# Kernel tuning notes

Hardware: AMD Instinct MI355X
Metric: run time of the kernel (lower is better)

The kernel has to match this reference:

```python
import jax, jax.numpy as jnp
import numpy as np

N = 50000    # num_nodes
E = 800000   # num_edges
IN = 256     # input_dim
H = 256      # hidden_dim
EPS = 1e-5   # BatchNorm eps


def setup_inputs() -> dict:
    key = jax.random.key(0)
    ks = jax.random.split(key, 12)
    def nrm(k, shp, s=0.05):
        return jax.random.normal(k, shp, dtype=jnp.float32) * s
    return {
        "x": jax.random.normal(ks[0], (N, IN), dtype=jnp.float32),
        "edge_index": jax.random.randint(ks[1], (2, E), 0, N, dtype=jnp.int32),
        "edge_weight": jax.random.uniform(ks[2], (E,), dtype=jnp.float32),
        # GCNConv 1 / 2 (PyG stores weight as [in, out]; bias [out])
        "W1": nrm(ks[3], (IN, H)), "b1": jnp.zeros((H,), jnp.float32),
        "W2": nrm(ks[4], (H, H)), "b2": jnp.zeros((H,), jnp.float32),
        # BatchNorm1d 1 / 2
        "gamma1": jnp.ones((H,), jnp.float32), "beta1": jnp.zeros((H,), jnp.float32),
        "gamma2": jnp.ones((H,), jnp.float32), "beta2": jnp.zeros((H,), jnp.float32),
        # LSTM 1 (input 2H) and LSTM 2 (input H), PyTorch gate order i,f,g,o
        "Wih1": nrm(ks[5], (4 * H, 2 * H)), "Whh1": nrm(ks[6], (4 * H, H)),
        "bih1": jnp.zeros((4 * H,), jnp.float32), "bhh1": jnp.zeros((4 * H,), jnp.float32),
        "Wih2": nrm(ks[7], (4 * H, H)), "Whh2": nrm(ks[8], (4 * H, H)),
        "bih2": jnp.zeros((4 * H,), jnp.float32), "bhh2": jnp.zeros((4 * H,), jnp.float32),
    }


def reference(x, edge_index, edge_weight, W1, b1, W2, b2, gamma1, beta1,
              gamma2, beta2, Wih1, Whh1, bih1, bhh1, Wih2, Whh2, bih2, bhh2):
    src, dst = edge_index[0], edge_index[1]
    # GCN symmetric normalization with added self-loops (fill value 1.0)
    loops = jnp.arange(N, dtype=src.dtype)
    src_a = jnp.concatenate([src, loops])
    dst_a = jnp.concatenate([dst, loops])
    ew_a = jnp.concatenate([edge_weight, jnp.ones((N,), edge_weight.dtype)])
    deg = jax.ops.segment_sum(ew_a, dst_a, num_segments=N)
    deg_safe = jnp.where(deg > 0, deg, 1.0)
    dinv = jnp.where(deg > 0, jax.lax.rsqrt(deg_safe), 0.0)
    norm = dinv[src_a] * ew_a * dinv[dst_a]  # [E+N]

    def gcn(h, W, b):
        m = (h @ W)[src_a] * norm[:, None]               # gather + scale messages
        return jax.ops.segment_sum(m, dst_a, num_segments=N) + b

    def bn(h, g, bta):  # training-mode BatchNorm1d (batch stats, biased var)
        mu = jnp.mean(h, axis=0)
        var = jnp.mean((h - mu) ** 2, axis=0)
        return (h - mu) * jax.lax.rsqrt(var + EPS) * g + bta

    def lstm_step0(inp, Wih, bih, bhh):  # single step from h0=c0=0 (window=1)
        gates = inp @ Wih.T + bih + bhh  # Whh term vanishes since h0=0
        i, f, g, o = jnp.split(gates, 4, axis=-1)
        c = jax.nn.sigmoid(i) * jnp.tanh(g)  # f*c0 = 0
        return jax.nn.sigmoid(o) * jnp.tanh(c)

    h1 = bn(jax.nn.relu(gcn(x, W1, b1)), gamma1, beta1)   # [N, H]
    h2 = bn(jax.nn.relu(gcn(h1, W2, b2)), gamma2, beta2)  # [N, H]
    Xc = jnp.concatenate([h1, h2], axis=1)                # [N, 2H]
    hL1 = lstm_step0(Xc, Wih1, bih1, bhh1)                # LSTM1 final hidden
    hL2 = lstm_step0(hL1, Wih2, bih2, bhh2)               # LSTM2 final hidden
    # S with window=1 reduces to x itself
    return jnp.concatenate([hL1, hL2, x], axis=1)         # [N, 2H + IN]
```

## Files before the change

### kernel.cpp

```cpp
#include <hip/hip_runtime.h>
#include <math.h>

#define NN 50000
#define NE 800000

typedef __attribute__((ext_vector_type(8))) short bf8;
typedef __attribute__((ext_vector_type(4))) float f32x4;
typedef unsigned int u32;
typedef unsigned long long u64;

__device__ __forceinline__ unsigned short f2b(float f){
  union{float f;unsigned u;} v; v.f=f;
  unsigned r=v.u+0x7fff+((v.u>>16)&1u);
  return (unsigned short)(r>>16);
}
__device__ __forceinline__ float b2f(unsigned short h){
  union{unsigned u;float f;} v; v.u=((unsigned)h)<<16; return v.f;
}
__device__ __forceinline__ float lo_bf(u32 t){ union{u32 u;float f;} v; v.u=t<<16; return v.f; }
__device__ __forceinline__ float hi_bf(u32 t){ union{u32 u;float f;} v; v.u=t&0xffff0000u; return v.f; }
__device__ __forceinline__ float fsigm(float x){ return __builtin_amdgcn_rcpf(1.f+__expf(-x)); }
__device__ __forceinline__ float ftanh(float x){ return 1.f-2.f*__builtin_amdgcn_rcpf(__expf(2.f*x)+1.f); }

__device__ __forceinline__ void gload16(const unsigned short* g, unsigned short* l){
  __builtin_amdgcn_global_load_lds((const __attribute__((address_space(1))) u32*)g,
                                   (__attribute__((address_space(3))) u32*)l,
                                   16,0,0);
}

__device__ __forceinline__ int wscan_incl(int v,int lane){
  #pragma unroll
  for(int d=1;d<64;d<<=1){ int t=__shfl_up(v,d,64); if(lane>=d)v+=t; }
  return v;
}

__global__ __launch_bounds__(256) void k_init(float* deg,int* cnt,float* colsum,float* colsq){
  int i=blockIdx.x*256+threadIdx.x;
  if(i<NN){deg[i]=1.0f;cnt[i]=0;}
  if(i<256){colsum[i]=0.f;colsq[i]=0.f;}
}

__global__ __launch_bounds__(256) void k_deg(const int* __restrict__ ei,const float* __restrict__ ew,
                                             float* deg,int* cnt){
  int e=blockIdx.x*256+threadIdx.x;
  if(e<NE){int d=ei[NE+e];atomicAdd(&deg[d],ew[e]);atomicAdd(&cnt[d],1);}
}

__global__ __launch_bounds__(256) void k_dinv(const float* __restrict__ deg,float* dinv){
  int i=blockIdx.x*256+threadIdx.x;
  if(i<NN){float d=deg[i];dinv[i]=d>0.f?rsqrtf(d):0.f;}
}

__global__ __launch_bounds__(1024) void k_scan1(const int* __restrict__ cnt,int* row_ptr,int* bsum){
  __shared__ int wsum[16];
  __shared__ int woff[17];
  int tid=threadIdx.x,lane=tid&63,w=tid>>6;
  int i=blockIdx.x*1024+tid;
  int v=(i<NN)?cnt[i]:0;
  int incl=wscan_incl(v,lane);
  if(lane==63)wsum[w]=incl;
  __syncthreads();
  if(w==0){
    int t=(lane<16)?wsum[lane]:0;
    int s=wscan_incl(t,lane);
    if(lane<16)woff[lane+1]=s;
    if(lane==0)woff[0]=0;
  }
  __syncthreads();
  int excl=incl-v+woff[w];
  if(i<NN)row_ptr[i]=excl;
  if(tid==0)bsum[blockIdx.x]=woff[16];
}
__global__ __launch_bounds__(64) void k_scan2(int* bsum,int* bbase,int* row_ptr,int nblk){
  int tid=threadIdx.x;
  int v=(tid<nblk)?bsum[tid]:0;
  int incl=wscan_incl(v,tid);
  bbase[tid]=incl-v;
  if(tid==63)row_ptr[NN]=incl;
}
__global__ __launch_bounds__(256) void k_scan3(int* row_ptr,int* cursor,const int* __restrict__ bbase){
  int i=blockIdx.x*256+threadIdx.x;
  if(i<NN){
    int r=row_ptr[i]+bbase[i>>10];
    row_ptr[i]=r;cursor[i]=r;
  }
}

__global__ __launch_bounds__(256) void k_scatter(const int* __restrict__ ei,const float* __restrict__ ew,
    const float* __restrict__ dinv,int* cursor,int2* csr_sw){
  int e=blockIdx.x*256+threadIdx.x;
  if(e<NE){
    int s=ei[e],d=ei[NE+e];
    float wv=dinv[s]*ew[e]*dinv[d];
    int p=atomicAdd(&cursor[d],1);
    int2 o;o.x=s;o.y=__float_as_int(wv);
    csr_sw[p]=o;
  }
}

__global__ __launch_bounds__(256) void k_wt(const float* __restrict__ W,unsigned short* __restrict__ Wt){
  int j=blockIdx.x,k=threadIdx.x;
  Wt[j*256+k]=f2b(W[k*256+j]);
}
__global__ __launch_bounds__(256) void k_f2b(const float* __restrict__ s,unsigned short* __restrict__ d,int n){
  int i=blockIdx.x*256+threadIdx.x;
  if(i<n)d[i]=f2b(s[i]);
}
__global__ __launch_bounds__(256) void k_cast(const float* __restrict__ s,unsigned short* __restrict__ d){
  long i=(long)blockIdx.x*256+threadIdx.x;
  float4 v=*(const float4*)&s[i*4];
  ushort4 o;o.x=f2b(v.x);o.y=f2b(v.y);o.z=f2b(v.z);o.w=f2b(v.w);
  *(ushort4*)&d[i*4]=o;
}
__global__ __launch_bounds__(256) void k_bsum(const float* __restrict__ a,const float* __restrict__ b,
                                              float* __restrict__ s,int n){
  int i=blockIdx.x*256+threadIdx.x;
  if(i<n)s[i]=a[i]+b[i];
}

__global__ __launch_bounds__(256) void k_foldw(const float* __restrict__ W,
    const float* __restrict__ scale,const float* __restrict__ shift,
    unsigned short* __restrict__ Wt,float* __restrict__ tw){
  __shared__ float red[256];
  int j=blockIdx.x,k=threadIdx.x;
  float w=W[k*256+j];
  Wt[j*256+k]=f2b(w*scale[k]);
  red[k]=w*shift[k];
  __syncthreads();
  for(int off=128;off>0;off>>=1){ if(k<off)red[k]+=red[k+off]; __syncthreads(); }
  if(k==0)tw[j]=red[0];
}

__global__ __launch_bounds__(256) void k_foldlstm(const float* __restrict__ Wih,int K,
    const float* __restrict__ scale,const float* __restrict__ shift,
    const float* __restrict__ bih,const float* __restrict__ bhh,
    unsigned short* __restrict__ Wb,float* __restrict__ bs){
  __shared__ float red[256];
  int m=blockIdx.x,t=threadIdx.x;
  float part=0.f;
  for(int k=t;k<K;k+=256){
    float w=Wih[(long)m*K+k];
    Wb[(long)m*K+k]=f2b(w*scale[k]);
    part+=w*shift[k];
  }
  red[t]=part;
  __syncthreads();
  for(int off=128;off>0;off>>=1){ if(t<off)red[t]+=red[t+off]; __syncthreads(); }
  if(t==0)bs[m]=bih[m]+bhh[m]+red[0];
}

__global__ __launch_bounds__(256,2) void k_gemm_mfma(
    const unsigned short* __restrict__ A,int lda,const unsigned short* __restrict__ Bt,int K,
    unsigned short* __restrict__ Cb){
  __shared__ unsigned short As[2][4096];
  __shared__ unsigned short Bs[2][4096];
  int tid=threadIdx.x;
  int row0=blockIdx.x*128,col0=blockIdx.y*128;
  int lane=tid&63,l15=lane&15,quad=lane>>4;
  int wid=tid>>6,wm=wid>>1,wn=wid&1;
  int sr=tid>>2;
  int aoff=((tid&3)^((tid>>3)&3))*8;
  int xq=quad^((l15>>1)&3);
  long ar0=row0+sr;    if(ar0>=NN)ar0=NN-1;
  long ar1=row0+64+sr; if(ar1>=NN)ar1=NN-1;
  const unsigned short* a0p=A+ar0*lda+aoff;
  const unsigned short* a1p=A+ar1*lda+aoff;
  const unsigned short* b0p=Bt+(long)(col0+sr)*K+aoff;
  const unsigned short* b1p=Bt+(long)(col0+64+sr)*K+aoff;
  int lb=wid*512;
  f32x4 acc[4][4]={};
  int nt=K/32;
  gload16(a0p,&As[0][lb]); gload16(a1p,&As[0][2048+lb]);
  gload16(b0p,&Bs[0][lb]); gload16(b1p,&Bs[0][2048+lb]);
  __syncthreads();
  for(int t=0;t<nt;t++){
    int cur=t&1;
    if(t+1<nt){
      int k0=(t+1)*32;int nxt=cur^1;
      gload16(a0p+k0,&As[nxt][lb]); gload16(a1p+k0,&As[nxt][2048+lb]);
      gload16(b0p+k0,&Bs[nxt][lb]); gload16(b1p+k0,&Bs[nxt][2048+lb]);
    }
    bf8 af[4],bfg[4];
    #pragma unroll
    for(int i=0;i<4;i++){
      af[i] =*(const bf8*)&As[cur][(wm*64+i*16+l15)*32+xq*8];
      bfg[i]=*(const bf8*)&Bs[cur][(wn*64+i*16+l15)*32+xq*8];
    }
    #pragma unroll
    for(int mi=0;mi<4;mi++)
      #pragma unroll
      for(int ni=0;ni<4;ni++)
        acc[mi][ni]=__builtin_amdgcn_mfma_f32_16x16x32_bf16(af[mi],bfg[ni],acc[mi][ni],0,0,0);
    __syncthreads();
  }
  #pragma unroll
  for(int mi=0;mi<4;mi++){
    #pragma unroll
    for(int r=0;r<4;r++){
      int node=row0+wm*64+mi*16+quad*4+r;
      if(node>=NN)continue;
      #pragma unroll
      for(int ni=0;ni<4;ni++){
        int col=col0+wn*64+ni*16+l15;
        Cb[((size_t)(col>>5)*NN+node)*32+(col&31)]=f2b(acc[mi][ni][r]);
      }
    }
  }
}

__global__ __launch_bounds__(256,2) void k_lstm_mfma(
    const unsigned short* __restrict__ A,int lda,int K,
    const unsigned short* __restrict__ Wb,const float* __restrict__ bsum,
    float* __restrict__ Hout,int ldh,unsigned short* __restrict__ Hb){
  __shared__ unsigned short As[2][4096];
  __shared__ unsigned short Bs[2][6144];
  int tid=threadIdx.x;
  int row0=blockIdx.x*128,m0=blockIdx.y*64;
  int lane=tid&63,l15=lane&15,quad=lane>>4;
  int wid=tid>>6,wm=wid>>1,wn=wid&1;
  int sr=tid>>2;
  int aoff=((tid&3)^((tid>>3)&3))*8;
  int xq=quad^((l15>>1)&3);
  long ar0=row0+sr;    if(ar0>=NN)ar0=NN-1;
  long ar1=row0+64+sr; if(ar1>=NN)ar1=NN-1;
  const unsigned short* a0p=A+ar0*lda+aoff;
  const unsigned short* a1p=A+ar1*lda+aoff;
  const unsigned short* wip=Wb+(long)(    m0+sr)*K+aoff;
  const unsigned short* wgp=Wb+(long)(512+m0+sr)*K+aoff;
  const unsigned short* wop=Wb+(long)(768+m0+sr)*K+aoff;
  int lb=wid*512;
  f32x4 ai[4][2]={},ag[4][2]={},ao[4][2]={};
  int nt=K/32;
  gload16(a0p,&As[0][lb]); gload16(a1p,&As[0][2048+lb]);
  gload16(wip,&Bs[0][lb]); gload16(wgp,&Bs[0][2048+lb]); gload16(wop,&Bs[0][4096+lb]);
  __syncthreads();
  for(int t=0;t<nt;t++){
    int cur=t&1;
    if(t+1<nt){
      int k0=(t+1)*32;int nxt=cur^1;
      gload16(a0p+k0,&As[nxt][lb]); gload16(a1p+k0,&As[nxt][2048+lb]);
      gload16(wip+k0,&Bs[nxt][lb]); gload16(wgp+k0,&Bs[nxt][2048+lb]); gload16(wop+k0,&Bs[nxt][4096+lb]);
    }
    bf8 af[4],bi[2],bg[2],bo[2];
    #pragma unroll
    for(int i=0;i<4;i++)af[i]=*(const bf8*)&As[cur][(wm*64+i*16+l15)*32+xq*8];
    #pragma unroll
    for(int ni=0;ni<2;ni++){
      int rr=wn*32+ni*16+l15;
      bi[ni]=*(const bf8*)&Bs[cur][(    rr)*32+xq*8];
      bg[ni]=*(const bf8*)&Bs[cur][( 64+rr)*32+xq*8];
      bo[ni]=*(const bf8*)&Bs[cur][(128+rr)*32+xq*8];
    }
    #pragma unroll
    for(int mi=0;mi<4;mi++)
      #pragma unroll
      for(int ni=0;ni<2;ni++){
        ai[mi][ni]=__builtin_amdgcn_mfma_f32_16x16x32_bf16(af[mi],bi[ni],ai[mi][ni],0,0,0);
        ag[mi][ni]=__builtin_amdgcn_mfma_f32_16x16x32_bf16(af[mi],bg[ni],ag[mi][ni],0,0,0);
        ao[mi][ni]=__builtin_amdgcn_mfma_f32_16x16x32_bf16(af[mi],bo[ni],ao[mi][ni],0,0,0);
      }
    __syncthreads();
  }
  #pragma unroll
  for(int ni=0;ni<2;ni++){
    int m=m0+wn*32+ni*16+l15;
    float b_i=bsum[m],b_g=bsum[512+m],b_o=bsum[768+m];
    #pragma unroll
    for(int mi=0;mi<4;mi++){
      #pragma unroll
      for(int r=0;r<4;r++){
        int node=row0+wm*64+mi*16+quad*4+r;
        if(node>=NN)continue;
        float gi=ai[mi][ni][r]+b_i;
        float gg=ag[mi][ni][r]+b_g;
        float go=ao[mi][ni][r]+b_o;
        float c=fsigm(gi)*ftanh(gg);
        float h=fsigm(go)*ftanh(c);
        Hout[(long)node*ldh+m]=h;
        if(Hb)Hb[(long)node*256+m]=f2b(h);
      }
    }
  }
}

__global__ __launch_bounds__(256) void k_spmm8(const unsigned short* __restrict__ T8,
    const int* __restrict__ row_ptr,const int2* __restrict__ csr_sw,
    const float* __restrict__ dinv,const float* __restrict__ bias,const float* __restrict__ tw,
    unsigned short* __restrict__ Xb,float* colsum,float* colsq){
  __shared__ float4 s_red[4][16];
  int tid=threadIdx.x;
  int lane=tid&63,wv=tid>>6;
  int g=lane>>4,li=lane&15;
  int chunk=blockIdx.x&7;
  int rowblk=blockIdx.x>>3;
  int r=rowblk*16+wv*4+g;
  int li2=li*2;
  int c0=chunk*32+li2;
  const unsigned short* Tc=T8+(size_t)chunk*NN*32;
  int p0=row_ptr[r],p1=row_ptr[r+1];
  int len=p1-p0;
  float di=dinv[r],ws=di*di;
  float rs=ws;
  u32 ts=*(const u32*)&Tc[(size_t)r*32+li2];
  float acc0=ws*lo_bf(ts),acc1=ws*hi_bf(ts);
  int Lm=len;
  Lm=max(Lm,__shfl_xor(Lm,16,64));
  Lm=max(Lm,__shfl_xor(Lm,32,64));
  for(int j=0;j<Lm;j+=4){
    #pragma unroll
    for(int u=0;u<4;u++){
      int jj=j+u;
      bool act=jj<len;
      int idx=p0+(act?jj:0);
      idx=min(idx,NE-1);
      u64 ev=__builtin_nontemporal_load((const u64*)&csr_sw[idx]);
      int s=(int)(u32)ev;
      float wgt=act?__int_as_float((int)(ev>>32)):0.f;
      s=min(max(s,0),NN-1);
      u32 t=*(const u32*)&Tc[(size_t)s*32+li2];
      acc0+=wgt*lo_bf(t);
      acc1+=wgt*hi_bf(t);
      rs+=wgt;
    }
  }
  float tw0=0.f,tw1=0.f;
  if(tw){ float2 tc=*(const float2*)&tw[c0]; tw0=tc.x; tw1=tc.y; }
  float2 bc=*(const float2*)&bias[c0];
  float a0=fmaxf(acc0+rs*tw0+bc.x,0.f);
  float a1=fmaxf(acc1+rs*tw1+bc.y,0.f);
  u32 o=(u32)f2b(a0)|((u32)f2b(a1)<<16);
  __builtin_nontemporal_store(o,(u32*)&Xb[(size_t)r*512+c0]);
  float s0=a0,s1=a1,q0=a0*a0,q1=a1*a1;
  #pragma unroll
  for(int m=16;m<=32;m<<=1){
    s0+=__shfl_xor(s0,m,64); s1+=__shfl_xor(s1,m,64);
    q0+=__shfl_xor(q0,m,64); q1+=__shfl_xor(q1,m,64);
  }
  if(lane<16)s_red[wv][lane]=make_float4(s0,s1,q0,q1);
  __syncthreads();
  if(tid<16){
    float4 a=s_red[0][tid],b=s_red[1][tid],c=s_red[2][tid],d=s_red[3][tid];
    float f0=a.x+b.x+c.x+d.x;
    float f1=a.y+b.y+c.y+d.y;
    float f2=a.z+b.z+c.z+d.z;
    float f3=a.w+b.w+c.w+d.w;
    int cc=chunk*32+tid*2;
    atomicAdd(&colsum[cc],f0);atomicAdd(&colsum[cc+1],f1);
    atomicAdd(&colsq[cc],f2);atomicAdd(&colsq[cc+1],f3);
  }
}

__global__ __launch_bounds__(256) void k_bnfin(const float* __restrict__ gamma,const float* __restrict__ beta,
    float* colsum,float* colsq,float* scale,float* shift){
  int c=threadIdx.x;
  float mu=colsum[c]/(float)NN;
  float var=colsq[c]/(float)NN-mu*mu;
  float r=rsqrtf(var+1e-5f);
  float sc=r*gamma[c];
  scale[c]=sc;
  shift[c]=beta[c]-mu*sc;
  colsum[c]=0.f;colsq[c]=0.f;
}

__global__ __launch_bounds__(256) void k_copy_out(const float* __restrict__ src,
    float* __restrict__ out,int colofs){
  long idx=(long)blockIdx.x*256+threadIdx.x;
  long r=idx>>6;int cc=(int)(idx&63)*4;
  if(r<NN)*(float4*)&out[r*768+colofs+cc]=*(const float4*)&src[r*256+cc];
}

extern "C" void kernel_launch(void* const* d_in,const int* in_sizes,int n_in,
                              void* d_out,int out_size,void* d_ws,size_t ws_size,
                              hipStream_t stream){
  const float* x   =(const float*)d_in[0];
  const int*   ei  =(const int*)  d_in[1];
  const float* ew  =(const float*)d_in[2];
  const float* W1  =(const float*)d_in[3];
  const float* b1  =(const float*)d_in[4];
  const float* W2  =(const float*)d_in[5];
  const float* b2  =(const float*)d_in[6];
  const float* g1  =(const float*)d_in[7];
  const float* be1 =(const float*)d_in[8];
  const float* g2  =(const float*)d_in[9];
  const float* be2 =(const float*)d_in[10];
  const float* Wih1=(const float*)d_in[11];
  const float* bih1=(const float*)d_in[13];
  const float* bhh1=(const float*)d_in[14];
  const float* Wih2=(const float*)d_in[15];
  const float* bih2=(const float*)d_in[17];
  const float* bhh2=(const float*)d_in[18];
  float* out=(float*)d_out;

  char* w=(char*)d_ws;
  auto alloc=[&](size_t bytes)->char*{char* p=w;w+=(bytes+255)&~(size_t)255;return p;};
  float* deg    =(float*)alloc((size_t)NN*4);
  float* dinv   =(float*)alloc((size_t)NN*4);
  int*   cnt    =(int*)  alloc((size_t)NN*4);
  int*   row_ptr=(int*)  alloc((size_t)(NN+1)*4);
  int*   cursor =(int*)  alloc((size_t)NN*4);
  int2*  csr_sw =(int2*) alloc((size_t)NE*8);
  int*   bsum_s =(int*)  alloc(64*4);
  int*   bbase  =(int*)  alloc(64*4);
  float* colsum =(float*)alloc(256*4);
  float* colsq  =(float*)alloc(256*4);
  float* scale  =(float*)alloc(512*4);
  float* shift  =(float*)alloc(512*4);
  float* tw     =(float*)alloc(256*4);
  unsigned short* Xcb =(unsigned short*)alloc((size_t)NN*512*2);
  unsigned short* TbH =(unsigned short*)alloc((size_t)NN*256*2);
  unsigned short* xb  =(unsigned short*)alloc((size_t)NN*256*2);
  unsigned short* Wt1 =(unsigned short*)alloc(256*256*2);
  unsigned short* Wt2 =(unsigned short*)alloc(256*256*2);
  unsigned short* Wb1 =(unsigned short*)alloc((size_t)1024*512*2);
  unsigned short* Wb2 =(unsigned short*)alloc((size_t)1024*256*2);
  float* bs1 =(float*)alloc(1024*4);
  float* bs2 =(float*)alloc(1024*4);

  int nb=(NN+255)/256;
  int nsc=(NN+1023)/1024;
  k_init<<<nb,256,0,stream>>>(deg,cnt,colsum,colsq);
  k_deg<<<(NE+255)/256,256,0,stream>>>(ei,ew,deg,cnt);
  k_dinv<<<nb,256,0,stream>>>(deg,dinv);
  k_scan1<<<nsc,1024,0,stream>>>(cnt,row_ptr,bsum_s);
  k_scan2<<<1,64,0,stream>>>(bsum_s,bbase,row_ptr,nsc);
  k_scan3<<<nb,256,0,stream>>>(row_ptr,cursor,bbase);
  k_scatter<<<(NE+255)/256,256,0,stream>>>(ei,ew,dinv,cursor,csr_sw);

  k_wt<<<256,256,0,stream>>>(W1,Wt1);
  k_cast<<<12500,256,0,stream>>>(x,xb);
  k_f2b<<<(1024*256+255)/256,256,0,stream>>>(Wih2,Wb2,1024*256);
  k_bsum<<<4,256,0,stream>>>(bih2,bhh2,bs2,1024);

  int ngx=(NN+127)/128;
  dim3 gd(ngx,2);
  dim3 gl(ngx,4);
  int nspmm=8*(NN/16);

  k_gemm_mfma<<<gd,256,0,stream>>>(xb,256,Wt1,256,TbH);
  k_spmm8<<<nspmm,256,0,stream>>>(TbH,row_ptr,csr_sw,dinv,b1,nullptr,Xcb+0,colsum,colsq);
  k_bnfin<<<1,256,0,stream>>>(g1,be1,colsum,colsq,scale,shift);
  k_foldw<<<256,256,0,stream>>>(W2,scale,shift,Wt2,tw);
  k_gemm_mfma<<<gd,256,0,stream>>>(Xcb,512,Wt2,256,TbH);
  k_spmm8<<<nspmm,256,0,stream>>>(TbH,row_ptr,csr_sw,dinv,b2,tw,Xcb+256,colsum,colsq);
  k_bnfin<<<1,256,0,stream>>>(g2,be2,colsum,colsq,scale+256,shift+256);
  k_foldlstm<<<1024,256,0,stream>>>(Wih1,512,scale,shift,bih1,bhh1,Wb1,bs1);
  k_lstm_mfma<<<gl,256,0,stream>>>(Xcb,512,512,Wb1,bs1,out+0,768,TbH);
  k_lstm_mfma<<<gl,256,0,stream>>>(TbH,256,256,Wb2,bs2,out+256,768,nullptr);
  k_copy_out<<<12500,256,0,stream>>>(x,out,512);
}
```

Baseline: 884.7 us.

## Widen SpMM gather to 16-byte loads with four lanes per row

```diff
diff --git a/kernel.cpp b/kernel.cpp
--- a/kernel.cpp
+++ b/kernel.cpp
@@ -17,8 +17,6 @@
 __device__ __forceinline__ float b2f(unsigned short h){
   union{unsigned u;float f;} v; v.u=((unsigned)h)<<16; return v.f;
 }
-__device__ __forceinline__ float lo_bf(u32 t){ union{u32 u;float f;} v; v.u=t<<16; return v.f; }
-__device__ __forceinline__ float hi_bf(u32 t){ union{u32 u;float f;} v; v.u=t&0xffff0000u; return v.f; }
 __device__ __forceinline__ float fsigm(float x){ return __builtin_amdgcn_rcpf(1.f+__expf(-x)); }
 __device__ __forceinline__ float ftanh(float x){ return 1.f-2.f*__builtin_amdgcn_rcpf(__expf(2.f*x)+1.f); }
 
@@ -287,66 +285,88 @@
     const int* __restrict__ row_ptr,const int2* __restrict__ csr_sw,
     const float* __restrict__ dinv,const float* __restrict__ bias,const float* __restrict__ tw,
     unsigned short* __restrict__ Xb,float* colsum,float* colsq){
-  __shared__ float4 s_red[4][16];
+  __shared__ float s_sum[4][32];
+  __shared__ float s_sq[4][32];
   int tid=threadIdx.x;
   int lane=tid&63,wv=tid>>6;
-  int g=lane>>4,li=lane&15;
+  int g=lane>>2,li=lane&3;
   int chunk=blockIdx.x&7;
   int rowblk=blockIdx.x>>3;
-  int r=rowblk*16+wv*4+g;
-  int li2=li*2;
-  int c0=chunk*32+li2;
+  int r=rowblk*64+wv*16+g;
+  bool valid=r<NN;
+  int rc=valid?r:0;
+  int co=li*8;
+  int c0=chunk*32+co;
   const unsigned short* Tc=T8+(size_t)chunk*NN*32;
-  int p0=row_ptr[r],p1=row_ptr[r+1];
-  int len=p1-p0;
-  float di=dinv[r],ws=di*di;
+  int p0=row_ptr[rc],p1=row_ptr[rc+1];
+  int len=valid?(p1-p0):0;
+  float di=dinv[rc],ws=di*di;
   float rs=ws;
-  u32 ts=*(const u32*)&Tc[(size_t)r*32+li2];
-  float acc0=ws*lo_bf(ts),acc1=ws*hi_bf(ts);
-  int Lm=len;
-  Lm=max(Lm,__shfl_xor(Lm,16,64));
-  Lm=max(Lm,__shfl_xor(Lm,32,64));
-  for(int j=0;j<Lm;j+=4){
-    #pragma unroll
-    for(int u=0;u<4;u++){
-      int jj=j+u;
-      bool act=jj<len;
-      int idx=p0+(act?jj:0);
-      idx=min(idx,NE-1);
-      u64 ev=__builtin_nontemporal_load((const u64*)&csr_sw[idx]);
-      int s=(int)(u32)ev;
-      float wgt=act?__int_as_float((int)(ev>>32)):0.f;
-      s=min(max(s,0),NN-1);
-      u32 t=*(const u32*)&Tc[(size_t)s*32+li2];
-      acc0+=wgt*lo_bf(t);
-      acc1+=wgt*hi_bf(t);
-      rs+=wgt;
-    }
-  }
-  float tw0=0.f,tw1=0.f;
-  if(tw){ float2 tc=*(const float2*)&tw[c0]; tw0=tc.x; tw1=tc.y; }
-  float2 bc=*(const float2*)&bias[c0];
-  float a0=fmaxf(acc0+rs*tw0+bc.x,0.f);
-  float a1=fmaxf(acc1+rs*tw1+bc.y,0.f);
-  u32 o=(u32)f2b(a0)|((u32)f2b(a1)<<16);
-  __builtin_nontemporal_store(o,(u32*)&Xb[(size_t)r*512+c0]);
-  float s0=a0,s1=a1,q0=a0*a0,q1=a1*a1;
+  float acc[8];
+  { bf8 t=*(const bf8*)&Tc[(u32)rc*32+co];
+    #pragma unroll
+    for(int e=0;e<8;e++)acc[e]=ws*b2f((unsigned short)t[e]);
+  }
+  int j=0;
+  for(;j+2<=len;j+=2){
+    u64 ev0=__builtin_nontemporal_load((const u64*)&csr_sw[p0+j]);
+    u64 ev1=__builtin_nontemporal_load((const u64*)&csr_sw[p0+j+1]);
+    int s0=(int)(u32)ev0; float w0=__int_as_float((int)(ev0>>32));
+    int s1=(int)(u32)ev1; float w1=__int_as_float((int)(ev1>>32));
+    s0=min(max(s0,0),NN-1); s1=min(max(s1,0),NN-1);
+    bf8 t0=*(const bf8*)&Tc[(u32)s0*32+co];
+    bf8 t1=*(const bf8*)&Tc[(u32)s1*32+co];
+    #pragma unroll
+    for(int e=0;e<8;e++)acc[e]+=w0*b2f((unsigned short)t0[e]);
+    #pragma unroll
+    for(int e=0;e<8;e++)acc[e]+=w1*b2f((unsigned short)t1[e]);
+    rs+=w0+w1;
+  }
+  if(j<len){
+    u64 ev=__builtin_nontemporal_load((const u64*)&csr_sw[p0+j]);
+    int s=(int)(u32)ev; float wg=__int_as_float((int)(ev>>32));
+    s=min(max(s,0),NN-1);
+    bf8 t=*(const bf8*)&Tc[(u32)s*32+co];
+    #pragma unroll
+    for(int e=0;e<8;e++)acc[e]+=wg*b2f((unsigned short)t[e]);
+    rs+=wg;
+  }
+  float4 bA=*(const float4*)&bias[c0],bB=*(const float4*)&bias[c0+4];
+  float4 tA=make_float4(0.f,0.f,0.f,0.f),tB=tA;
+  if(tw){ tA=*(const float4*)&tw[c0]; tB=*(const float4*)&tw[c0+4]; }
+  float o[8];
+  o[0]=fmaxf(acc[0]+rs*tA.x+bA.x,0.f);
+  o[1]=fmaxf(acc[1]+rs*tA.y+bA.y,0.f);
+  o[2]=fmaxf(acc[2]+rs*tA.z+bA.z,0.f);
+  o[3]=fmaxf(acc[3]+rs*tA.w+bA.w,0.f);
+  o[4]=fmaxf(acc[4]+rs*tB.x+bB.x,0.f);
+  o[5]=fmaxf(acc[5]+rs*tB.y+bB.y,0.f);
+  o[6]=fmaxf(acc[6]+rs*tB.z+bB.z,0.f);
+  o[7]=fmaxf(acc[7]+rs*tB.w+bB.w,0.f);
+  if(valid){
+    bf8 ov;
+    #pragma unroll
+    for(int e=0;e<8;e++)ov[e]=(short)f2b(o[e]);
+    __builtin_nontemporal_store(ov,(bf8*)&Xb[(size_t)r*512+c0]);
+  }
+  float sv[8],qv[8];
   #pragma unroll
-  for(int m=16;m<=32;m<<=1){
-    s0+=__shfl_xor(s0,m,64); s1+=__shfl_xor(s1,m,64);
-    q0+=__shfl_xor(q0,m,64); q1+=__shfl_xor(q1,m,64);
-  }
-  if(lane<16)s_red[wv][lane]=make_float4(s0,s1,q0,q1);
-  __syncthreads();
-  if(tid<16){
-    float4 a=s_red[0][tid],b=s_red[1][tid],c=s_red[2][tid],d=s_red[3][tid];
-    float f0=a.x+b.x+c.x+d.x;
-    float f1=a.y+b.y+c.y+d.y;
-    float f2=a.z+b.z+c.z+d.z;
-    float f3=a.w+b.w+c.w+d.w;
-    int cc=chunk*32+tid*2;
-    atomicAdd(&colsum[cc],f0);atomicAdd(&colsum[cc+1],f1);
-    atomicAdd(&colsq[cc],f2);atomicAdd(&colsq[cc+1],f3);
+  for(int e=0;e<8;e++){ float v=valid?o[e]:0.f; sv[e]=v; qv[e]=v*v; }
+  #pragma unroll
+  for(int m=4;m<64;m<<=1){
+    #pragma unroll
+    for(int e=0;e<8;e++){ sv[e]+=__shfl_xor(sv[e],m,64); qv[e]+=__shfl_xor(qv[e],m,64); }
+  }
+  if(g==0){
+    #pragma unroll
+    for(int e=0;e<8;e++){ s_sum[wv][co+e]=sv[e]; s_sq[wv][co+e]=qv[e]; }
+  }
+  __syncthreads();
+  if(tid<32){
+    float a=s_sum[0][tid]+s_sum[1][tid]+s_sum[2][tid]+s_sum[3][tid];
+    float q=s_sq[0][tid]+s_sq[1][tid]+s_sq[2][tid]+s_sq[3][tid];
+    atomicAdd(&colsum[chunk*32+tid],a);
+    atomicAdd(&colsq[chunk*32+tid],q);
   }
 }
 
@@ -434,7 +454,7 @@
   int ngx=(NN+127)/128;
   dim3 gd(ngx,2);
   dim3 gl(ngx,4);
-  int nspmm=8*(NN/16);
+  int nspmm=8*((NN+63)/64);
 
   k_gemm_mfma<<<gd,256,0,stream>>>(xb,256,Wt1,256,TbH);
   k_spmm8<<<nspmm,256,0,stream>>>(TbH,row_ptr,csr_sw,dinv,b1,nullptr,Xcb+0,colsum,colsq);
```

New measurement: 779.8 us. 11.9% less time.
